# Performance work log

Measured on AMD Instinct MI355X. Metric: run time of the kernel, lower is better.

The kernel has to match this reference:

```python
import jax, jax.numpy as jnp
import numpy as np

EPS = 1e-7
ROUTINGS = 3


def squash(s, axis=-1):
    # norm over `axis`; faithful to torch: (|s|^2/(1+|s|^2)) * (s/(|s|+eps))
    norm = jnp.linalg.norm(s, axis=axis, keepdims=True)
    sq = norm * norm
    return (sq / (1.0 + sq)) * (s / (norm + EPS))


def conv2d(x, w, b, stride):
    y = jax.lax.conv_general_dilated(
        x, w, window_strides=(stride, stride), padding='VALID',
        dimension_numbers=('NCHW', 'OIHW', 'NCHW'))
    return y + b[None, :, None, None]


def setup_inputs() -> dict:
    key = jax.random.key(0)
    ks = jax.random.split(key, 12)
    B = 256
    return {
        'x': jax.random.normal(ks[0], (B, 1, 28, 28), dtype=jnp.float32),
        'conv1_w': 0.05 * jax.random.normal(ks[1], (256, 1, 9, 9), dtype=jnp.float32),
        'conv1_b': jnp.zeros((256,), jnp.float32),
        'conv2_w': 0.02 * jax.random.normal(ks[2], (256, 256, 9, 9), dtype=jnp.float32),
        'conv2_b': jnp.zeros((256,), jnp.float32),
        'W_caps': 0.01 * jax.random.normal(ks[3], (10, 1152, 16, 8), dtype=jnp.float32),
        'dec_w1': 0.05 * jax.random.normal(ks[4], (160, 512), dtype=jnp.float32),
        'dec_b1': jnp.zeros((512,), jnp.float32),
        'dec_w2': 0.04 * jax.random.normal(ks[5], (512, 1024), dtype=jnp.float32),
        'dec_b2': jnp.zeros((1024,), jnp.float32),
        'dec_w3': 0.03 * jax.random.normal(ks[6], (1024, 784), dtype=jnp.float32),
        'dec_b3': jnp.zeros((784,), jnp.float32),
    }


def reference(x, conv1_w, conv1_b, conv2_w, conv2_b, W_caps,
              dec_w1, dec_b1, dec_w2, dec_b2, dec_w3, dec_b3):
    B = x.shape[0]
    # conv1: [B,1,28,28] -> [B,256,20,20]
    h = conv2d(x, conv1_w, conv1_b, stride=1)
    # primary capsules: conv -> [B,256,6,6]
    h = conv2d(h, conv2_w, conv2_b, stride=2)
    # faithful to original: squash over the LAST spatial axis (dim=-1)
    h = squash(h, axis=-1)
    u = h.reshape(B, -1, 8)  # [B,1152,8]

    # u_hat[b,o,i,d] = W_caps[o,i,d,e] @ u[b,i,e]  -> [B,10,1152,16]
    u_hat = jnp.einsum('oide,bie->boid', W_caps, u)
    u_hat_det = jax.lax.stop_gradient(u_hat)

    b_logits = jnp.zeros((B, 10, 1152), u_hat.dtype)
    for it in range(ROUTINGS):
        c = jax.nn.softmax(b_logits, axis=1)  # over output capsules
        if it == ROUTINGS - 1:
            v = squash(jnp.sum(c[:, :, :, None] * u_hat, axis=-2, keepdims=True))
        else:
            v = squash(jnp.sum(c[:, :, :, None] * u_hat_det, axis=-2, keepdims=True))
            b_logits = b_logits + jnp.sum(v * u_hat_det, axis=-1)
    v = jnp.squeeze(v, axis=-2)  # [B,10,16]

    length = jnp.linalg.norm(v, axis=-1)  # [B,10]
    # y defaults to one-hot of argmax(length), constant w.r.t. grads
    y = jax.lax.stop_gradient(
        jax.nn.one_hot(jnp.argmax(length, axis=1), 10, dtype=v.dtype))
    masked = (v * y[:, :, None]).reshape(B, -1)  # [B,160]
    h1 = jax.nn.relu(masked @ dec_w1 + dec_b1)
    h2 = jax.nn.relu(h1 @ dec_w2 + dec_b2)
    reconstruction = jax.nn.sigmoid(h2 @ dec_w3 + dec_b3)  # [B,784]
    return length, reconstruction
```

## Files before the change

kernel.cpp:

```cpp
#include <hip/hip_runtime.h>
#include <cstdint>
#include <cstddef>

typedef __bf16 bf16x8 __attribute__((ext_vector_type(8)));
typedef short  shortx8 __attribute__((ext_vector_type(8)));
typedef float  floatx4 __attribute__((ext_vector_type(4)));
typedef float  floatx2 __attribute__((ext_vector_type(2)));
typedef float  floatx16 __attribute__((ext_vector_type(16)));
typedef int    intx4v __attribute__((ext_vector_type(4)));
typedef int    intx8 __attribute__((ext_vector_type(8)));
typedef unsigned short ushort8 __attribute__((ext_vector_type(8)));
typedef unsigned short ushort4v __attribute__((ext_vector_type(4)));

__device__ __forceinline__ float bflo(unsigned int u) {
    union { unsigned int u32; float f; } x; x.u32 = u << 16; return x.f;
}
__device__ __forceinline__ float bfhi(unsigned int u) {
    union { unsigned int u32; float f; } x; x.u32 = u & 0xffff0000u; return x.f;
}
__device__ __forceinline__ unsigned short f2bf(float f) {
    union { float f; unsigned int u; } x; x.f = f;
    unsigned int u = x.u;
    unsigned int r = (u + 0x7fffu + ((u >> 16) & 1u)) >> 16;
    return (unsigned short)r;
}
__device__ __forceinline__ unsigned char f2fp8(float f) {
    unsigned int pk = __builtin_amdgcn_cvt_pk_fp8_f32(f, f, 0, false);
    return (unsigned char)(pk & 0xff);
}
__device__ __forceinline__ void fp8x4_dec(unsigned int u, float* f) {
    floatx2 lo = __builtin_amdgcn_cvt_pk_f32_fp8(u, false);
    floatx2 hi = __builtin_amdgcn_cvt_pk_f32_fp8(u, true);
    f[0] = lo[0]; f[1] = lo[1]; f[2] = hi[0]; f[3] = hi[1];
}

#define GLOBAL_U32 const __attribute__((address_space(1))) unsigned int*
#define LDS_U32 __attribute__((address_space(3))) unsigned int*
__device__ __forceinline__ void async_cp16(const void* g, void* l) {
    __builtin_amdgcn_global_load_lds((GLOBAL_U32)g, (LDS_U32)l, 16, 0, 0);
}

#define UHAT_SCALE 64.0f
#define UHAT_INV   (1.0f / 64.0f)
#define W2_SCALE   16.0f
#define W2_INV     (1.0f / 16.0f)

__global__ __launch_bounds__(256) void prep_k(const float* __restrict__ x,
                                              const float* __restrict__ w1c,
                                              const float* __restrict__ b1c,
                                              const float* __restrict__ w2,
                                              unsigned char* __restrict__ h1t8,
                                              unsigned char* __restrict__ w2t8,
                                              float* __restrict__ S012) {
    const int blk = blockIdx.x, t = threadIdx.x;
    if (t < 120) S012[blk * 120 + t] = 0.f;
    if (blk < 512) {
        __shared__ float xs[1024];
        __shared__ unsigned short wb[96 * 132];
        const int b = blk >> 1, ch0 = (blk & 1) * 128;
        for (int i = t; i < 1024; i += 256) xs[i] = (i < 784) ? x[b * 784 + i] : 0.f;
        for (int i = t; i < 96 * 132; i += 256) wb[i] = 0;
        __syncthreads();
        for (int i = t; i < 81 * 128; i += 256) {
            const int tap = i >> 7, chl = i & 127;
            wb[tap * 132 + chl] = f2bf(w1c[(size_t)(ch0 + chl) * 81 + tap]);
        }
        __syncthreads();
        const int lane = t & 63, l15 = lane & 15, g = lane >> 4;
        const int wave = t >> 6;
        const int n0l = wave * 32;
        int xoff[3][8];
#pragma unroll
        for (int kk = 0; kk < 3; ++kk)
#pragma unroll
            for (int e = 0; e < 8; ++e) {
                const int tap = kk * 32 + g * 8 + e;
                const int kh = tap / 9, kw = tap - 9 * kh;
                xoff[kk][e] = kh * 28 + kw;
            }
        shortx8 bF[2][3];
#pragma unroll
        for (int nt = 0; nt < 2; ++nt)
#pragma unroll
            for (int kk = 0; kk < 3; ++kk) {
                shortx8 v;
#pragma unroll
                for (int e = 0; e < 8; ++e) {
                    const int tap = kk * 32 + g * 8 + e;
                    v[e] = (short)wb[tap * 132 + n0l + nt * 16 + l15];
                }
                bF[nt][kk] = v;
            }
        float bv[2][4];
#pragma unroll
        for (int nt = 0; nt < 2; ++nt)
#pragma unroll
            for (int r = 0; r < 4; ++r)
                bv[nt][r] = b1c[ch0 + n0l + nt * 16 + g * 4 + r];
        for (int mt = 0; mt < 25; ++mt) {
            const int s = mt * 16 + l15;
            const int oh = s / 20, ow = s - 20 * oh;
            const int s2 = oh * 28 + ow;
            shortx8 aF[3];
#pragma unroll
            for (int kk = 0; kk < 3; ++kk) {
                shortx8 v;
#pragma unroll
                for (int e = 0; e < 8; ++e) v[e] = (short)f2bf(xs[s2 + xoff[kk][e]]);
                aF[kk] = v;
            }
            const size_t sbase = ((size_t)(b * 20 + oh) * 20 + ow) * 256 + ch0 + n0l + g * 4;
#pragma unroll
            for (int nt = 0; nt < 2; ++nt) {
                floatx4 acc = (floatx4){0.f, 0.f, 0.f, 0.f};
#pragma unroll
                for (int kk = 0; kk < 3; ++kk)
                    acc = __builtin_amdgcn_mfma_f32_16x16x32_bf16(bF[nt][kk], aF[kk], acc, 0, 0, 0);
                unsigned int w = 0;
                w = __builtin_amdgcn_cvt_pk_fp8_f32(acc[0] + bv[nt][0], acc[1] + bv[nt][1], w, false);
                w = __builtin_amdgcn_cvt_pk_fp8_f32(acc[2] + bv[nt][2], acc[3] + bv[nt][3], w, true);
                *(unsigned int*)(h1t8 + sbase + nt * 16) = w;
            }
        }
    } else {
        __shared__ float shm[10368];
        const int id = blk - 512;
        const int oc = id >> 1, half = id & 1;
        const float* src = w2 + (size_t)oc * 20736 + half * 128 * 81;
        for (int idx = t; idx < 10368; idx += 256) shm[idx] = src[idx];
        __syncthreads();
        unsigned char* dst = w2t8 + (size_t)oc * 20736 + half * 128;
        for (int idx = t; idx < 10368; idx += 256) {
            const int tap = idx >> 7, icl = idx & 127;
            dst[tap * 256 + icl] = f2fp8(shm[icl * 81 + tap] * W2_SCALE);
        }
    }
}

__device__ __forceinline__ int c2_rowbase(int m) {
    const int b = m / 36, sp = m % 36;
    const int oh = sp / 6, ow = sp % 6;
    return (b * 400 + oh * 40 + ow * 2) * 256;
}

__global__ __launch_bounds__(256) void conv2_k(const unsigned char* __restrict__ h1t8,
                                               const unsigned char* __restrict__ w2t8,
                                               unsigned short* __restrict__ part) {
    const int t = threadIdx.x;
    const int id = blockIdx.x;
    const int G = id >> 4;
    const int bx = (id >> 3) & 1;
    const int s = id & 7;
    const int by = 2 * G + (s >> 2);
    const int z  = ((s & 3) + by) & 3;
    __shared__ unsigned char At[128 * 128];
    __shared__ unsigned char Bt[128 * 128];

    const int oc0 = bx * 128;

    int aRB[4], bBase[4];
#pragma unroll
    for (int k = 0; k < 4; ++k) {
        const int a = t + 256 * k;
        const int r = a >> 3, sg = a & 7;
        const int u = sg ^ (r & 7);
        aRB[k] = c2_rowbase(by * 128 + r) + u * 16;
        bBase[k] = (oc0 + r) * 20736 + u * 16;
    }

    const int lane = t & 63, l31 = lane & 31, h = lane >> 5;
    const int wave = t >> 6;
    const int wM = (wave & 1) * 64, wOC = (wave >> 1) * 64;

    int aO[2][2][2], bO[2][2][2];
#pragma unroll
    for (int i = 0; i < 2; ++i) {
        const int Ra = wOC + i * 32 + l31;
        const int Rb = wM + i * 32 + l31;
#pragma unroll
        for (int st = 0; st < 2; ++st)
#pragma unroll
            for (int p = 0; p < 2; ++p) {
                const int c = st * 4 + h * 2 + p;
                aO[st][i][p] = Ra * 128 + ((c ^ (Ra & 7)) << 4);
                bO[st][i][p] = Rb * 128 + ((c ^ (Rb & 7)) << 4);
            }
    }

    floatx16 acc[2][2];
#pragma unroll
    for (int i = 0; i < 2; ++i)
#pragma unroll
        for (int j = 0; j < 2; ++j)
#pragma unroll
            for (int r = 0; r < 16; ++r) acc[i][j][r] = 0.f;

    const int q0 = (162 * z) >> 2, q1 = (162 * (z + 1)) >> 2;
    for (int q = q0; q < q1; ++q) {
        const int tap = q >> 1;
        const int kh = tap / 9, kw = tap - 9 * kh;
        const int aoffB = (kh * 20 + kw) * 256 + (q & 1) * 128;
        __syncthreads();
#pragma unroll
        for (int k = 0; k < 4; ++k)
            async_cp16(h1t8 + aRB[k] + aoffB, At + (t + 256 * k) * 16);
#pragma unroll
        for (int k = 0; k < 4; ++k)
            async_cp16(w2t8 + bBase[k] + q * 128, Bt + (t + 256 * k) * 16);
        __syncthreads();
#pragma unroll
        for (int st = 0; st < 2; ++st) {
            intx8 aF[2], bF[2];
#pragma unroll
            for (int i = 0; i < 2; ++i) {
                const intx4v alo = *(const intx4v*)(Bt + aO[st][i][0]);
                const intx4v ahi = *(const intx4v*)(Bt + aO[st][i][1]);
                aF[i] = (intx8){alo[0], alo[1], alo[2], alo[3], ahi[0], ahi[1], ahi[2], ahi[3]};
                const intx4v blo = *(const intx4v*)(At + bO[st][i][0]);
                const intx4v bhi = *(const intx4v*)(At + bO[st][i][1]);
                bF[i] = (intx8){blo[0], blo[1], blo[2], blo[3], bhi[0], bhi[1], bhi[2], bhi[3]};
            }
#pragma unroll
            for (int i = 0; i < 2; ++i)
#pragma unroll
                for (int j = 0; j < 2; ++j)
                    acc[i][j] = __builtin_amdgcn_mfma_scale_f32_32x32x64_f8f6f4(
                        aF[i], bF[j], acc[i][j], 0, 0, 0, 127, 0, 127);
        }
    }

    unsigned short* pz = part + (size_t)z * 2359296;
#pragma unroll
    for (int i = 0; i < 2; ++i) {
#pragma unroll
        for (int j = 0; j < 2; ++j) {
            const int m = by * 128 + wM + j * 32 + l31;
#pragma unroll
            for (int rg = 0; rg < 4; ++rg) {
                const int oc = oc0 + wOC + i * 32 + rg * 8 + 4 * h;
                ushort4v pk;
#pragma unroll
                for (int rr = 0; rr < 4; ++rr) pk[rr] = f2bf(acc[i][j][rg * 4 + rr] * W2_INV);
                *(ushort4v*)(pz + (size_t)m * 256 + oc) = pk;
            }
        }
    }
}

__global__ __launch_bounds__(256) void squash_u_k(const unsigned short* __restrict__ part,
                                                  const float* __restrict__ bias,
                                                  float* __restrict__ u) {
    const int bb = blockIdx.x, t = threadIdx.x;
    const int b = bb >> 1, h = bb & 1;
    __shared__ float hs[4608];
    const size_t base = (size_t)b * 9216 + h * 4608;
    for (int q = t; q < 2304; q += 256) {
        const int idx = q * 2;
        float v0 = bias[idx & 255], v1 = bias[(idx + 1) & 255];
#pragma unroll
        for (int z = 0; z < 4; ++z) {
            const unsigned int uu = *(const unsigned int*)(part + (size_t)z * 2359296 + base + idx);
            v0 += bflo(uu);
            v1 += bfhi(uu);
        }
        hs[idx] = v0; hs[idx + 1] = v1;
    }
    __syncthreads();
    for (int gq = t; gq < 768; gq += 256) {
        const int c = gq / 3, ohl = gq % 3;
        const int oh = h * 3 + ohl;
        float s[6], sq = 0.f;
#pragma unroll
        for (int ow = 0; ow < 6; ++ow) { s[ow] = hs[(ohl * 6 + ow) * 256 + c]; sq = fmaf(s[ow], s[ow], sq); }
        const float norm = sqrtf(sq);
        const float f = (sq / (1.0f + sq)) / (norm + 1e-7f);
        float* up = u + (size_t)b * 9216 + c * 36 + oh * 6;
#pragma unroll
        for (int ow = 0; ow < 6; ++ow) up[ow] = s[ow] * f;
    }
}

__global__ __launch_bounds__(256) void uhat_k(const float* __restrict__ Wc,
                                              const float* __restrict__ u,
                                              unsigned int* __restrict__ uhat8) {
    const int i = blockIdx.x, t = threadIdx.x;
    __shared__ float Wl[1280];
    for (int idx = t; idx < 1280; idx += 256) {
        const int o = idx >> 7, r = idx & 127;
        Wl[idx] = Wc[((size_t)o * 1152 + i) * 128 + r];
    }
    float ur[8];
    *(float4*)&ur[0] = *(const float4*)(u + (size_t)t * 9216 + i * 8);
    *(float4*)&ur[4] = *(const float4*)(u + (size_t)t * 9216 + i * 8 + 4);
    __syncthreads();
    unsigned int* row = uhat8 + ((size_t)i * 256 + t) * 40;
#pragma unroll 1
    for (int o = 0; o < 10; ++o) {
        float vals[16];
#pragma unroll
        for (int d = 0; d < 16; ++d) {
            const float* wp = &Wl[o * 128 + d * 8];
            float a = 0.f;
#pragma unroll
            for (int e = 0; e < 8; ++e) a = fmaf(wp[e], ur[e], a);
            vals[d] = a * UHAT_SCALE;
        }
        uint4 pk;
        unsigned int w;
#pragma unroll
        for (int q = 0; q < 4; ++q) {
            w = 0;
            w = __builtin_amdgcn_cvt_pk_fp8_f32(vals[q * 4 + 0], vals[q * 4 + 1], w, false);
            w = __builtin_amdgcn_cvt_pk_fp8_f32(vals[q * 4 + 2], vals[q * 4 + 3], w, true);
            if (q == 0) pk.x = w; else if (q == 1) pk.y = w; else if (q == 2) pk.z = w; else pk.w = w;
        }
        *(uint4*)(row + o * 4) = pk;
    }
}

__global__ __launch_bounds__(256) void route_iter0_k(const unsigned int* __restrict__ uhat8,
                                                     float* __restrict__ S0) {
    const int b = blockIdx.x, i0 = blockIdx.y * 128, t = threadIdx.x;
    __shared__ __align__(16) unsigned int Ul8[128 * 40];
    const unsigned int* ub = uhat8 + ((size_t)i0 * 256 + b) * 40;
#pragma unroll
    for (int rep = 0; rep < 5; ++rep) {
        const int c = rep * 256 + t;
        const int row = c / 10, q = c - row * 10;
        async_cp16(ub + (size_t)row * 10240 + q * 4, (char*)Ul8 + c * 16);
    }
    __syncthreads();
    const int th = t & 127, hi = t >> 7;
    if (th < 40) {
        const unsigned int* p = Ul8 + hi * 64 * 40 + th;
        float a0 = 0.f, a1 = 0.f, a2 = 0.f, a3 = 0.f;
#pragma unroll 4
        for (int i = 0; i < 64; ++i) {
            float f[4];
            fp8x4_dec(p[i * 40], f);
            a0 += f[0]; a1 += f[1]; a2 += f[2]; a3 += f[3];
        }
        const float sc = 0.1f * UHAT_INV;
        atomicAdd(&S0[b * 160 + 4 * th + 0], sc * a0);
        atomicAdd(&S0[b * 160 + 4 * th + 1], sc * a1);
        atomicAdd(&S0[b * 160 + 4 * th + 2], sc * a2);
        atomicAdd(&S0[b * 160 + 4 * th + 3], sc * a3);
    }
}

template <int ITER>
__global__ __launch_bounds__(256) void route_iter_k(const unsigned int* __restrict__ uhat8,
                                                    const float* __restrict__ S_in,
                                                    float* __restrict__ BL,
                                                    float* __restrict__ S_out) {
    const int b = blockIdx.x, i0 = blockIdx.y * 128, t = threadIdx.x;
    __shared__ __align__(16) unsigned int Ul8[128 * 40];
    __shared__ float Vl[160];
    __shared__ float cT[10 * 132];
    __shared__ float dots[128 * 10];

    const unsigned int* ub = uhat8 + ((size_t)i0 * 256 + b) * 40;
#pragma unroll
    for (int rep = 0; rep < 5; ++rep) {
        const int c = rep * 256 + t;
        const int row = c / 10, q = c - row * 10;
        async_cp16(ub + (size_t)row * 10240 + q * 4, (char*)Ul8 + c * 16);
    }

    if (t < 160) {
        const float x = S_in[b * 160 + t];
        float sq = x * x;
        sq += __shfl_xor(sq, 1, 16);
        sq += __shfl_xor(sq, 2, 16);
        sq += __shfl_xor(sq, 4, 16);
        sq += __shfl_xor(sq, 8, 16);
        const float norm = sqrtf(sq);
        const float f = (sq / (1.f + sq)) / (norm + 1e-7f);
        Vl[t] = x * f;
    }
    __syncthreads();

    const int o = t % 10, s = t / 10;
    float vr[16];
    if (t < 250) {
#pragma unroll
        for (int q = 0; q < 4; ++q)
            *(float4*)&vr[q * 4] = *(const float4*)(&Vl[o * 16 + q * 4]);
    }

    if (t < 250) {
#pragma unroll
        for (int rep = 0; rep < 6; ++rep) {
            const int i = s + 25 * rep;
            if (i < 128) {
                const uint4 uu = *(const uint4*)(Ul8 + i * 40 + o * 4);
                float f[16];
                fp8x4_dec(uu.x, f);
                fp8x4_dec(uu.y, f + 4);
                fp8x4_dec(uu.z, f + 8);
                fp8x4_dec(uu.w, f + 12);
                float dot = 0.f;
#pragma unroll
                for (int d = 0; d < 16; ++d) dot = fmaf(f[d], vr[d], dot);
                dots[i * 10 + o] = dot * UHAT_INV;
            }
        }
    }
    __syncthreads();

    if (t < 128) {
        float bl[10];
#pragma unroll
        for (int oo = 0; oo < 10; ++oo) bl[oo] = dots[t * 10 + oo];
        if (ITER == 2) {
#pragma unroll
            for (int oo = 0; oo < 10; ++oo) bl[oo] += BL[(size_t)b * 11520 + oo * 1152 + i0 + t];
        } else {
#pragma unroll
            for (int oo = 0; oo < 10; ++oo) BL[(size_t)b * 11520 + oo * 1152 + i0 + t] = bl[oo];
        }
        float mx = bl[0];
#pragma unroll
        for (int oo = 1; oo < 10; ++oo) mx = fmaxf(mx, bl[oo]);
        float ex[10], sum = 0.f;
#pragma unroll
        for (int oo = 0; oo < 10; ++oo) { ex[oo] = expf(bl[oo] - mx); sum += ex[oo]; }
        const float inv = 1.f / sum;
#pragma unroll
        for (int oo = 0; oo < 10; ++oo) cT[oo * 132 + t] = ex[oo] * inv;
    }
    __syncthreads();

    const int th = t & 127, hi = t >> 7;
    if (th < 40) {
        const int oq = th >> 2;
        const unsigned int* base = Ul8 + hi * 64 * 40 + th;
        const float* cb = &cT[oq * 132 + hi * 64];
        float a0 = 0.f, a1 = 0.f, a2 = 0.f, a3 = 0.f;
#pragma unroll 4
        for (int ii = 0; ii < 64; ++ii) {
            const float c = cb[ii];
            float f[4];
            fp8x4_dec(base[ii * 40], f);
            a0 = fmaf(c, f[0], a0);
            a1 = fmaf(c, f[1], a1);
            a2 = fmaf(c, f[2], a2);
            a3 = fmaf(c, f[3], a3);
        }
        atomicAdd(&S_out[b * 160 + 4 * th + 0], a0 * UHAT_INV);
        atomicAdd(&S_out[b * 160 + 4 * th + 1], a1 * UHAT_INV);
        atomicAdd(&S_out[b * 160 + 4 * th + 2], a2 * UHAT_INV);
        atomicAdd(&S_out[b * 160 + 4 * th + 3], a3 * UHAT_INV);
    }
}

__global__ __launch_bounds__(512) void final_k(const float* __restrict__ S,
                                               const float* __restrict__ w1,
                                               const float* __restrict__ b1,
                                               float* __restrict__ out_len,
                                               float* __restrict__ h1d) {
    const int b = blockIdx.x, t = threadIdx.x;
    __shared__ float v_s[160];
    __shared__ float len_s[10];
    __shared__ int sel_s;
    if (t < 160) {
        const float x = S[b * 160 + t];
        float sq = x * x;
        sq += __shfl_xor(sq, 1, 16);
        sq += __shfl_xor(sq, 2, 16);
        sq += __shfl_xor(sq, 4, 16);
        sq += __shfl_xor(sq, 8, 16);
        const float norm = sqrtf(sq);
        const float f = (sq / (1.f + sq)) / (norm + 1e-7f);
        v_s[t] = x * f;
        if ((t & 15) == 0) {
            const float len = f * norm;
            len_s[t >> 4] = len;
            out_len[b * 10 + (t >> 4)] = len;
        }
    }
    __syncthreads();
    if (t == 0) {
        float best = len_s[0]; int bi = 0;
        for (int oo = 1; oo < 10; ++oo) if (len_s[oo] > best) { best = len_s[oo]; bi = oo; }
        sel_s = bi;
    }
    __syncthreads();
    const int s = sel_s;
    float acc = b1[t];
    const float* wrow = w1 + (size_t)(s * 16) * 512 + t;
#pragma unroll
    for (int j = 0; j < 16; ++j) acc = fmaf(v_s[s * 16 + j], wrow[j * 512], acc);
    h1d[(size_t)b * 512 + t] = fmaxf(acc, 0.f);
}

template <int ACT>
__global__ __launch_bounds__(256) void mlp3_k(const float* __restrict__ A,
                                              const float* __restrict__ Bm,
                                              const float* __restrict__ bias,
                                              float* __restrict__ C, int N, int K) {
    extern __shared__ float Asm[];
    const int t = threadIdx.x;
    const int m0 = blockIdx.y * 8, n0 = blockIdx.x * 64;
    const int RS = K + 4;
    const int k4 = K >> 2;
    for (int i = t; i < 8 * k4; i += 256) {
        const int r = i / k4, c = i - r * k4;
        *(float4*)&Asm[r * RS + c * 4] = *(const float4*)&A[(size_t)(m0 + r) * K + c * 4];
    }
    __syncthreads();
    const int lane = t & 63, w = t >> 6;
    const int mq = lane >> 4, nq = lane & 15;
    const int n = n0 + nq * 4;
    const int ncl = (n + 3 < N) ? n : (N - 4);
    const float* bp = Bm + ncl;
    const float* asA = &Asm[(mq * 2 + 0) * RS];
    const float* asB = &Asm[(mq * 2 + 1) * RS];
    const int kQ = K >> 2;
    const int kBeg = w * kQ;
    const int nBat2 = kQ >> 4;
    float4 acc0 = {0.f, 0.f, 0.f, 0.f}, acc1 = {0.f, 0.f, 0.f, 0.f};
    float4 ba[8], bb[8];
#pragma unroll
    for (int d = 0; d < 8; ++d) ba[d] = *(const float4*)&bp[(size_t)(kBeg + d) * N];

#define MLP3_FMA(BATCH, KB)                                                       \
    _Pragma("unroll")                                                             \
    for (int d = 0; d < 8; ++d) {                                                 \
        const float4 b = BATCH[d];                                                \
        const float a0 = asA[(KB) + d];                                           \
        const float a1 = asB[(KB) + d];                                           \
        acc0.x = fmaf(a0, b.x, acc0.x); acc0.y = fmaf(a0, b.y, acc0.y);           \
        acc0.z = fmaf(a0, b.z, acc0.z); acc0.w = fmaf(a0, b.w, acc0.w);           \
        acc1.x = fmaf(a1, b.x, acc1.x); acc1.y = fmaf(a1, b.y, acc1.y);           \
        acc1.z = fmaf(a1, b.z, acc1.z); acc1.w = fmaf(a1, b.w, acc1.w);           \
    }

    int k = kBeg;
#pragma unroll 1
    for (int it = 0; it < nBat2; ++it) {
#pragma unroll
        for (int d = 0; d < 8; ++d) bb[d] = *(const float4*)&bp[(size_t)(k + 8 + d) * N];
        MLP3_FMA(ba, k)
        if (it + 1 < nBat2) {
#pragma unroll
            for (int d = 0; d < 8; ++d) ba[d] = *(const float4*)&bp[(size_t)(k + 16 + d) * N];
        }
        MLP3_FMA(bb, k + 8)
        k += 16;
    }
#undef MLP3_FMA

    __syncthreads();
    float* red = Asm;
    float* my = &red[(size_t)(w * 64 + lane) * 8];
    my[0] = acc0.x; my[1] = acc0.y; my[2] = acc0.z; my[3] = acc0.w;
    my[4] = acc1.x; my[5] = acc1.y; my[6] = acc1.z; my[7] = acc1.w;
    __syncthreads();
    if (t < 64) {
        float o[8];
#pragma unroll
        for (int x = 0; x < 8; ++x)
            o[x] = red[(size_t)t * 8 + x] + red[(size_t)(64 + t) * 8 + x]
                 + red[(size_t)(128 + t) * 8 + x] + red[(size_t)(192 + t) * 8 + x];
        const int nn = n0 + (t & 15) * 4;
#pragma unroll
        for (int rm = 0; rm < 2; ++rm) {
            const int m = m0 + (t >> 4) * 2 + rm;
#pragma unroll
            for (int rn = 0; rn < 4; ++rn) {
                const int ncol = nn + rn;
                if (ncol < N) {
                    float v = o[rm * 4 + rn] + bias[ncol];
                    if (ACT == 0) v = fmaxf(v, 0.f);
                    else v = 1.f / (1.f + expf(-v));
                    C[(size_t)m * N + ncol] = v;
                }
            }
        }
    }
}

extern "C" void kernel_launch(void* const* d_in, const int* in_sizes, int n_in,
                              void* d_out, int out_size, void* d_ws, size_t ws_size,
                              hipStream_t stream) {
    const float* x   = (const float*)d_in[0];
    const float* w1  = (const float*)d_in[1];
    const float* b1  = (const float*)d_in[2];
    const float* w2  = (const float*)d_in[3];
    const float* b2  = (const float*)d_in[4];
    const float* Wc  = (const float*)d_in[5];
    const float* dw1 = (const float*)d_in[6];
    const float* db1 = (const float*)d_in[7];
    const float* dw2 = (const float*)d_in[8];
    const float* db2 = (const float*)d_in[9];
    const float* dw3 = (const float*)d_in[10];
    const float* db3 = (const float*)d_in[11];
    float* out = (float*)d_out;

    char* ws = (char*)d_ws;
    unsigned char* H1T8 = (unsigned char*)(ws + 0);
    unsigned char* W2T8 = (unsigned char*)(ws + 26214400);
    unsigned short* PART = (unsigned short*)(ws + 31522816);
    unsigned int*   UHAT = (unsigned int*)(ws + 0);
    float* U    = (float*)(ws + 50397184);
    float* BL   = (float*)(ws + 59834368);
    float* S012 = (float*)(ws + 71630848);
    float* H1D  = (float*)(ws + 59834368);
    float* H2D  = (float*)(ws + 60358656);

    float* S0 = S012, *S1 = S012 + 40960, *S2 = S012 + 81920;

    prep_k<<<1024, 256, 0, stream>>>(x, w1, b1, w2, H1T8, W2T8, S012);
    conv2_k<<<576, 256, 0, stream>>>(H1T8, W2T8, PART);
    squash_u_k<<<512, 256, 0, stream>>>(PART, b2, U);
    uhat_k<<<1152, 256, 0, stream>>>(Wc, U, UHAT);
    route_iter0_k<<<dim3(256, 9), 256, 0, stream>>>(UHAT, S0);
    route_iter_k<1><<<dim3(256, 9), 256, 0, stream>>>(UHAT, S0, BL, S1);
    route_iter_k<2><<<dim3(256, 9), 256, 0, stream>>>(UHAT, S1, BL, S2);
    final_k<<<256, 512, 0, stream>>>(S2, dw1, db1, out, H1D);
    mlp3_k<0><<<dim3(16, 32), 256, 8 * 516 * 4, stream>>>(H1D, dw2, db2, H2D, 1024, 512);
    mlp3_k<1><<<dim3(13, 32), 256, 8 * 1028 * 4, stream>>>(H2D, dw3, db3, out + 2560, 784, 1024);
}
```

Measured before the change: 329.7 us.

## Fuse three routing iterations into one per-batch kernel with double-buffered uhat staging

Replaces the three routing kernels (each a 256x9 grid using atomics into S buffers) with a single kernel, one block per batch element. Each block loops over the nine 128-capsule chunks with double-buffered async LDS loads and reduces partial sums in shared memory instead of global atomics. This also removes the S012 zeroing in prep. uhat_k now stages its output in LDS and writes it out as coalesced 16-byte stores. The cost is only 256 blocks on a large GPU, reading uhat three times from global or L2 per block, and several more barriers per chunk.

Result: faster. 319.8 us (-3.0%).

```diff
diff --git a/kernel.cpp b/kernel.cpp
--- a/kernel.cpp
+++ b/kernel.cpp
@@ -50,10 +50,8 @@
                                               const float* __restrict__ b1c,
                                               const float* __restrict__ w2,
                                               unsigned char* __restrict__ h1t8,
-                                              unsigned char* __restrict__ w2t8,
-                                              float* __restrict__ S012) {
+                                              unsigned char* __restrict__ w2t8) {
     const int blk = blockIdx.x, t = threadIdx.x;
-    if (t < 120) S012[blk * 120 + t] = 0.f;
     if (blk < 512) {
         __shared__ float xs[1024];
         __shared__ unsigned short wb[96 * 132];
@@ -285,6 +283,7 @@
                                               unsigned int* __restrict__ uhat8) {
     const int i = blockIdx.x, t = threadIdx.x;
     __shared__ float Wl[1280];
+    __shared__ __align__(16) unsigned int Ust[256 * 40];
     for (int idx = t; idx < 1280; idx += 256) {
         const int o = idx >> 7, r = idx & 127;
         Wl[idx] = Wc[((size_t)o * 1152 + i) * 128 + r];
@@ -293,7 +292,7 @@
     *(float4*)&ur[0] = *(const float4*)(u + (size_t)t * 9216 + i * 8);
     *(float4*)&ur[4] = *(const float4*)(u + (size_t)t * 9216 + i * 8 + 4);
     __syncthreads();
-    unsigned int* row = uhat8 + ((size_t)i * 256 + t) * 40;
+    unsigned int* myrow = Ust + t * 40;
 #pragma unroll 1
     for (int o = 0; o < 10; ++o) {
         float vals[16];
@@ -314,143 +313,169 @@
             w = __builtin_amdgcn_cvt_pk_fp8_f32(vals[q * 4 + 2], vals[q * 4 + 3], w, true);
             if (q == 0) pk.x = w; else if (q == 1) pk.y = w; else if (q == 2) pk.z = w; else pk.w = w;
         }
-        *(uint4*)(row + o * 4) = pk;
-    }
-}
-
-__global__ __launch_bounds__(256) void route_iter0_k(const unsigned int* __restrict__ uhat8,
-                                                     float* __restrict__ S0) {
-    const int b = blockIdx.x, i0 = blockIdx.y * 128, t = threadIdx.x;
-    __shared__ __align__(16) unsigned int Ul8[128 * 40];
-    const unsigned int* ub = uhat8 + ((size_t)i0 * 256 + b) * 40;
-#pragma unroll
-    for (int rep = 0; rep < 5; ++rep) {
-        const int c = rep * 256 + t;
-        const int row = c / 10, q = c - row * 10;
-        async_cp16(ub + (size_t)row * 10240 + q * 4, (char*)Ul8 + c * 16);
-    }
-    __syncthreads();
-    const int th = t & 127, hi = t >> 7;
-    if (th < 40) {
-        const unsigned int* p = Ul8 + hi * 64 * 40 + th;
-        float a0 = 0.f, a1 = 0.f, a2 = 0.f, a3 = 0.f;
-#pragma unroll 4
-        for (int i = 0; i < 64; ++i) {
-            float f[4];
-            fp8x4_dec(p[i * 40], f);
-            a0 += f[0]; a1 += f[1]; a2 += f[2]; a3 += f[3];
-        }
-        const float sc = 0.1f * UHAT_INV;
-        atomicAdd(&S0[b * 160 + 4 * th + 0], sc * a0);
-        atomicAdd(&S0[b * 160 + 4 * th + 1], sc * a1);
-        atomicAdd(&S0[b * 160 + 4 * th + 2], sc * a2);
-        atomicAdd(&S0[b * 160 + 4 * th + 3], sc * a3);
-    }
-}
-
-template <int ITER>
-__global__ __launch_bounds__(256) void route_iter_k(const unsigned int* __restrict__ uhat8,
-                                                    const float* __restrict__ S_in,
-                                                    float* __restrict__ BL,
-                                                    float* __restrict__ S_out) {
-    const int b = blockIdx.x, i0 = blockIdx.y * 128, t = threadIdx.x;
-    __shared__ __align__(16) unsigned int Ul8[128 * 40];
+        *(uint4*)(myrow + o * 4) = pk;
+    }
+    __syncthreads();
+    unsigned int* gbase = uhat8 + (size_t)i * 10240;
+    for (int u2 = t; u2 < 2560; u2 += 256)
+        *(uint4*)(gbase + (size_t)u2 * 4) = *(const uint4*)(Ust + u2 * 4);
+}
+
+__global__ __launch_bounds__(256) void route_all_k(const unsigned int* __restrict__ uhat8,
+                                                   float* __restrict__ BL,
+                                                   float* __restrict__ S2out) {
+    const int b = blockIdx.x, t = threadIdx.x;
+    __shared__ __align__(16) unsigned int Ul8[2][128 * 40];
     __shared__ float Vl[160];
     __shared__ float cT[10 * 132];
     __shared__ float dots[128 * 10];
 
-    const unsigned int* ub = uhat8 + ((size_t)i0 * 256 + b) * 40;
-#pragma unroll
-    for (int rep = 0; rep < 5; ++rep) {
-        const int c = rep * 256 + t;
-        const int row = c / 10, q = c - row * 10;
-        async_cp16(ub + (size_t)row * 10240 + q * 4, (char*)Ul8 + c * 16);
-    }
-
+    const int seg = t / 80, rr = t - seg * 80;
+    const int hi = rr / 40, th = rr - hi * 40;
+    const int oq = th >> 2;
+    const bool p2act = (t < 240);
+    const int lo = (seg * 64) / 3, hiE = ((seg + 1) * 64) / 3;
+    const int o = t % 10, sidx = t / 10;
+
+    auto stage = [&](int buf, int chunk) {
+        const unsigned int* ub = uhat8 + ((size_t)(chunk * 128) * 256 + b) * 40;
+#pragma unroll
+        for (int rep = 0; rep < 5; ++rep) {
+            const int c = rep * 256 + t;
+            const int row = c / 10, q = c - row * 10;
+            async_cp16(ub + (size_t)row * 10240 + q * 4, (char*)Ul8[buf] + c * 16);
+        }
+    };
+
+    float a0 = 0.f, a1 = 0.f, a2 = 0.f, a3 = 0.f;
+    stage(0, 0);
+    __syncthreads();
+    for (int ck = 0; ck < 9; ++ck) {
+        const int cur = ck & 1;
+        if (ck + 1 < 9) stage(cur ^ 1, ck + 1);
+        if (p2act) {
+            const unsigned int* base = Ul8[cur] + hi * 64 * 40 + th;
+            for (int ii = lo; ii < hiE; ++ii) {
+                float f[4];
+                fp8x4_dec(base[ii * 40], f);
+                a0 += f[0]; a1 += f[1]; a2 += f[2]; a3 += f[3];
+            }
+        }
+        __syncthreads();
+    }
+    if (p2act) {
+        float* red = dots;
+        const int rb = seg * 320 + hi * 160 + 4 * th;
+        red[rb + 0] = a0; red[rb + 1] = a1; red[rb + 2] = a2; red[rb + 3] = a3;
+    }
+    __syncthreads();
     if (t < 160) {
-        const float x = S_in[b * 160 + t];
-        float sq = x * x;
+        const float xv = 0.1f * UHAT_INV *
+            (dots[t] + dots[160 + t] + dots[320 + t] + dots[480 + t] + dots[640 + t] + dots[800 + t]);
+        float sq = xv * xv;
         sq += __shfl_xor(sq, 1, 16);
         sq += __shfl_xor(sq, 2, 16);
         sq += __shfl_xor(sq, 4, 16);
         sq += __shfl_xor(sq, 8, 16);
         const float norm = sqrtf(sq);
         const float f = (sq / (1.f + sq)) / (norm + 1e-7f);
-        Vl[t] = x * f;
-    }
-    __syncthreads();
-
-    const int o = t % 10, s = t / 10;
-    float vr[16];
-    if (t < 250) {
-#pragma unroll
-        for (int q = 0; q < 4; ++q)
-            *(float4*)&vr[q * 4] = *(const float4*)(&Vl[o * 16 + q * 4]);
-    }
-
-    if (t < 250) {
-#pragma unroll
-        for (int rep = 0; rep < 6; ++rep) {
-            const int i = s + 25 * rep;
-            if (i < 128) {
-                const uint4 uu = *(const uint4*)(Ul8 + i * 40 + o * 4);
-                float f[16];
-                fp8x4_dec(uu.x, f);
-                fp8x4_dec(uu.y, f + 4);
-                fp8x4_dec(uu.z, f + 8);
-                fp8x4_dec(uu.w, f + 12);
-                float dot = 0.f;
-#pragma unroll
-                for (int d = 0; d < 16; ++d) dot = fmaf(f[d], vr[d], dot);
-                dots[i * 10 + o] = dot * UHAT_INV;
-            }
-        }
-    }
-    __syncthreads();
-
-    if (t < 128) {
-        float bl[10];
-#pragma unroll
-        for (int oo = 0; oo < 10; ++oo) bl[oo] = dots[t * 10 + oo];
-        if (ITER == 2) {
-#pragma unroll
-            for (int oo = 0; oo < 10; ++oo) bl[oo] += BL[(size_t)b * 11520 + oo * 1152 + i0 + t];
-        } else {
-#pragma unroll
-            for (int oo = 0; oo < 10; ++oo) BL[(size_t)b * 11520 + oo * 1152 + i0 + t] = bl[oo];
-        }
-        float mx = bl[0];
-#pragma unroll
-        for (int oo = 1; oo < 10; ++oo) mx = fmaxf(mx, bl[oo]);
-        float ex[10], sum = 0.f;
-#pragma unroll
-        for (int oo = 0; oo < 10; ++oo) { ex[oo] = expf(bl[oo] - mx); sum += ex[oo]; }
-        const float inv = 1.f / sum;
-#pragma unroll
-        for (int oo = 0; oo < 10; ++oo) cT[oo * 132 + t] = ex[oo] * inv;
-    }
-    __syncthreads();
-
-    const int th = t & 127, hi = t >> 7;
-    if (th < 40) {
-        const int oq = th >> 2;
-        const unsigned int* base = Ul8 + hi * 64 * 40 + th;
-        const float* cb = &cT[oq * 132 + hi * 64];
-        float a0 = 0.f, a1 = 0.f, a2 = 0.f, a3 = 0.f;
-#pragma unroll 4
-        for (int ii = 0; ii < 64; ++ii) {
-            const float c = cb[ii];
-            float f[4];
-            fp8x4_dec(base[ii * 40], f);
-            a0 = fmaf(c, f[0], a0);
-            a1 = fmaf(c, f[1], a1);
-            a2 = fmaf(c, f[2], a2);
-            a3 = fmaf(c, f[3], a3);
-        }
-        atomicAdd(&S_out[b * 160 + 4 * th + 0], a0 * UHAT_INV);
-        atomicAdd(&S_out[b * 160 + 4 * th + 1], a1 * UHAT_INV);
-        atomicAdd(&S_out[b * 160 + 4 * th + 2], a2 * UHAT_INV);
-        atomicAdd(&S_out[b * 160 + 4 * th + 3], a3 * UHAT_INV);
+        Vl[t] = xv * f;
+    }
+    __syncthreads();
+
+    for (int it = 1; it <= 2; ++it) {
+        float vr[16];
+        if (t < 250) {
+#pragma unroll
+            for (int q = 0; q < 4; ++q)
+                *(float4*)&vr[q * 4] = *(const float4*)(&Vl[o * 16 + q * 4]);
+        }
+        a0 = a1 = a2 = a3 = 0.f;
+        stage(0, 0);
+        __syncthreads();
+        for (int ck = 0; ck < 9; ++ck) {
+            const int cur = ck & 1;
+            if (ck + 1 < 9) stage(cur ^ 1, ck + 1);
+            if (t < 250) {
+#pragma unroll
+                for (int rep = 0; rep < 6; ++rep) {
+                    const int i = sidx + 25 * rep;
+                    if (i < 128) {
+                        const uint4 uu = *(const uint4*)(Ul8[cur] + i * 40 + o * 4);
+                        float f[16];
+                        fp8x4_dec(uu.x, f);
+                        fp8x4_dec(uu.y, f + 4);
+                        fp8x4_dec(uu.z, f + 8);
+                        fp8x4_dec(uu.w, f + 12);
+                        float dot = 0.f;
+#pragma unroll
+                        for (int d = 0; d < 16; ++d) dot = fmaf(f[d], vr[d], dot);
+                        dots[i * 10 + o] = dot * UHAT_INV;
+                    }
+                }
+            }
+            __syncthreads();
+            if (t < 128) {
+                float bl[10];
+#pragma unroll
+                for (int oo = 0; oo < 10; ++oo) bl[oo] = dots[t * 10 + oo];
+                const size_t blb = (size_t)b * 11520 + (size_t)ck * 128 + t;
+                if (it == 1) {
+#pragma unroll
+                    for (int oo = 0; oo < 10; ++oo) BL[blb + (size_t)oo * 1152] = bl[oo];
+                } else {
+#pragma unroll
+                    for (int oo = 0; oo < 10; ++oo) bl[oo] += BL[blb + (size_t)oo * 1152];
+                }
+                float mx = bl[0];
+#pragma unroll
+                for (int oo = 1; oo < 10; ++oo) mx = fmaxf(mx, bl[oo]);
+                float ex[10], sum = 0.f;
+#pragma unroll
+                for (int oo = 0; oo < 10; ++oo) { ex[oo] = expf(bl[oo] - mx); sum += ex[oo]; }
+                const float inv = 1.f / sum;
+#pragma unroll
+                for (int oo = 0; oo < 10; ++oo) cT[oo * 132 + t] = ex[oo] * inv;
+            }
+            __syncthreads();
+            if (p2act) {
+                const unsigned int* base = Ul8[cur] + hi * 64 * 40 + th;
+                const float* cb = &cT[oq * 132 + hi * 64];
+                for (int ii = lo; ii < hiE; ++ii) {
+                    const float c = cb[ii];
+                    float f[4];
+                    fp8x4_dec(base[ii * 40], f);
+                    a0 = fmaf(c, f[0], a0);
+                    a1 = fmaf(c, f[1], a1);
+                    a2 = fmaf(c, f[2], a2);
+                    a3 = fmaf(c, f[3], a3);
+                }
+            }
+            __syncthreads();
+        }
+        if (p2act) {
+            float* red = dots;
+            const int rb = seg * 320 + hi * 160 + 4 * th;
+            red[rb + 0] = a0; red[rb + 1] = a1; red[rb + 2] = a2; red[rb + 3] = a3;
+        }
+        __syncthreads();
+        if (t < 160) {
+            const float sv = UHAT_INV *
+                (dots[t] + dots[160 + t] + dots[320 + t] + dots[480 + t] + dots[640 + t] + dots[800 + t]);
+            if (it == 1) {
+                float sq = sv * sv;
+                sq += __shfl_xor(sq, 1, 16);
+                sq += __shfl_xor(sq, 2, 16);
+                sq += __shfl_xor(sq, 4, 16);
+                sq += __shfl_xor(sq, 8, 16);
+                const float norm = sqrtf(sq);
+                const float f = (sq / (1.f + sq)) / (norm + 1e-7f);
+                Vl[t] = sv * f;
+            } else {
+                S2out[b * 160 + t] = sv;
+            }
+        }
+        __syncthreads();
     }
 }
 
@@ -605,19 +630,15 @@
     unsigned int*   UHAT = (unsigned int*)(ws + 0);
     float* U    = (float*)(ws + 50397184);
     float* BL   = (float*)(ws + 59834368);
-    float* S012 = (float*)(ws + 71630848);
+    float* S2   = (float*)(ws + 71958528);
     float* H1D  = (float*)(ws + 59834368);
     float* H2D  = (float*)(ws + 60358656);
 
-    float* S0 = S012, *S1 = S012 + 40960, *S2 = S012 + 81920;
-
-    prep_k<<<1024, 256, 0, stream>>>(x, w1, b1, w2, H1T8, W2T8, S012);
+    prep_k<<<1024, 256, 0, stream>>>(x, w1, b1, w2, H1T8, W2T8);
     conv2_k<<<576, 256, 0, stream>>>(H1T8, W2T8, PART);
     squash_u_k<<<512, 256, 0, stream>>>(PART, b2, U);
     uhat_k<<<1152, 256, 0, stream>>>(Wc, U, UHAT);
-    route_iter0_k<<<dim3(256, 9), 256, 0, stream>>>(UHAT, S0);
-    route_iter_k<1><<<dim3(256, 9), 256, 0, stream>>>(UHAT, S0, BL, S1);
-    route_iter_k<2><<<dim3(256, 9), 256, 0, stream>>>(UHAT, S1, BL, S2);
+    route_all_k<<<256, 256, 0, stream>>>(UHAT, BL, S2);
     final_k<<<256, 512, 0, stream>>>(S2, dw1, db1, out, H1D);
     mlp3_k<0><<<dim3(16, 32), 256, 8 * 516 * 4, stream>>>(H1D, dw2, db2, H2D, 1024, 512);
     mlp3_k<1><<<dim3(13, 32), 256, 8 * 1028 * 4, stream>>>(H2D, dw3, db3, out + 2560, 784, 1024);
```
